# Kernel tuning notes

Measured on AMD Instinct MI355X. Metric: run time of the kernel, lower is better.

## Reference

```python
import jax, jax.numpy as jnp
import numpy as np

B, T, E, H = 8, 2048, 128, 4
FACTOR = 3  # autocorr_factor


def setup_inputs() -> dict:
    key = jax.random.key(0)
    ks = jax.random.split(key, 9)
    s = 0.05
    return {
        "hidden_states": jax.random.normal(ks[0], (B, T, E), jnp.float32),
        "wq": jax.random.normal(ks[1], (E, E, H), jnp.float32) * s,
        "bq": jax.random.normal(ks[2], (E, H), jnp.float32) * s,
        "wk": jax.random.normal(ks[3], (E, E, H), jnp.float32) * s,
        "bk": jax.random.normal(ks[4], (E, H), jnp.float32) * s,
        "wv": jax.random.normal(ks[5], (E, E, H), jnp.float32) * s,
        "bv": jax.random.normal(ks[6], (E, H), jnp.float32) * s,
        "wo": jax.random.normal(ks[7], (E, H, E), jnp.float32) * s,
        "bo": jax.random.normal(ks[8], (E,), jnp.float32) * s,
    }


def reference(hidden_states, wq, bq, wk, bk, wv, bv, wo, bo):
    # Inference path (training=None) of AutoCorrelation.call
    bsize, seq_len, _ = hidden_states.shape
    q = jnp.einsum('btj,juh->btuh', hidden_states, wq) + bq  # [B,T,E,H]
    k = jnp.einsum('btj,juh->btuh', hidden_states, wk) + bk
    v = jnp.einsum('btj,juh->btuh', hidden_states, wv) + bv

    # FFT cross-correlation over time axis
    qf = jnp.fft.rfft(q.transpose(0, 2, 3, 1), n=seq_len, axis=-1)  # [B,E,H,F]
    kf = jnp.fft.rfft(k.transpose(0, 2, 3, 1), n=seq_len, axis=-1)
    ac = jnp.fft.irfft(qf * jnp.conj(kf), n=seq_len, axis=-1)       # [B,E,H,T]
    ac = ac.transpose(0, 3, 1, 2)                                   # [B,T,E,H]

    ac_mean = ac.mean(axis=-1)                                      # [B,T,E]
    top_k = int(FACTOR * np.log(float(seq_len)))

    # top-k delays per (batch, channel)
    vals, idx = jax.lax.top_k(ac_mean.transpose(0, 2, 1), top_k)    # [B,E,K]
    w = jax.nn.softmax(vals, axis=-1)  # == Softmax(axis=-2) on [B,K,E]

    # NOTE: in the source, `delays_agg +=` is dedented outside the top_k loop,
    # so only the LAST iteration (i = top_k-1) contributes. Replicated faithfully.
    delay = idx[:, :, top_k - 1]   # [B,E] int
    wgt = w[:, :, top_k - 1]       # [B,E]

    # gather over doubled values == circular roll by -delay per (b, channel)
    t_idx = (jnp.arange(seq_len)[None, :, None] + delay[:, None, :]) % seq_len  # [B,T,E]
    rolled = jnp.take_along_axis(v, t_idx[..., None], axis=1)       # [B,T,E,H]
    agg = rolled * wgt[:, None, :, None]                            # [B,T,E,H]

    return jnp.einsum('btjh,jhf->btf', agg, wo) + bo                # [B,T,E]
```

## Files before the change

### kernel.cpp

```cpp
#include <hip/hip_runtime.h>
#include <math.h>

#define TSEQ 2048
#define BB 8
#define EE 128
#define HH 4
#define UHN 512
#define KTOP 22
#define BT (BB*TSEQ)
#define PITCH 76

typedef _Float16 f16;
typedef f16 f16x2 __attribute__((ext_vector_type(2)));
typedef f16 f16x4 __attribute__((ext_vector_type(4)));
typedef f16 f16x8 __attribute__((ext_vector_type(8)));
typedef float f32x4 __attribute__((ext_vector_type(4)));

__device__ __forceinline__ float2 cmul(float2 a, float2 b) {
  return make_float2(a.x*b.x - a.y*b.y, a.x*b.y + a.y*b.x);
}

__device__ __forceinline__ f16x8 ld_frag(const f16* p) {
  f16x4 lo = *(const f16x4*)(p);
  f16x4 hi = *(const f16x4*)(p + 16);
  return __builtin_shufflevector(lo, hi, 0, 1, 2, 3, 4, 5, 6, 7);
}

__global__ __launch_bounds__(256, 2)
void proj_mfma(const float* __restrict__ hs,
               const float* __restrict__ wq, const float* __restrict__ bq,
               const float* __restrict__ wk, const float* __restrict__ bk,
               const float* __restrict__ wv, const float* __restrict__ bv,
               float* __restrict__ q_t, float* __restrict__ k_t, float* __restrict__ v_t)
{
  __shared__ f16 Ah[128*PITCH];
  __shared__ f16 Al[128*PITCH];
  __shared__ f16 Bh[128*PITCH];
  __shared__ f16 Bl[128*PITCH];

  const float* W; const float* bias; float* outp;
  if (blockIdx.z == 0)      { W = wq; bias = bq; outp = q_t; }
  else if (blockIdx.z == 1) { W = wk; bias = bk; outp = k_t; }
  else                      { W = wv; bias = bv; outp = v_t; }

  const int tid  = threadIdx.x;
  const int lane = tid & 63, wid = tid >> 6;
  const int wm = wid >> 1, wn = wid & 1;
  const int ln15 = lane & 15, g = lane >> 4;
  const int uh0 = blockIdx.x * 128;
  const int bt0 = blockIdx.y * 128;

  f32x4 acc[4][4] = {};

  for (int kc = 0; kc < 2; ++kc) {
    const int k0 = kc * 64;
    __syncthreads();
#pragma unroll
    for (int r = 0; r < 16; ++r) {
      int idx = tid + 256*r;
      int u = idx & 127, kp = idx >> 7;
      float w0 = W[(size_t)(k0 + 2*kp    )*UHN + uh0 + u];
      float w1 = W[(size_t)(k0 + 2*kp + 1)*UHN + uh0 + u];
      f16 h0 = (f16)w0, h1 = (f16)w1;
      f16 l0 = (f16)(w0 - (float)h0), l1 = (f16)(w1 - (float)h1);
      *(f16x2*)&Ah[u*PITCH + 2*kp] = (f16x2){h0, h1};
      *(f16x2*)&Al[u*PITCH + 2*kp] = (f16x2){l0, l1};
    }
#pragma unroll
    for (int r = 0; r < 8; ++r) {
      int idx4 = tid + 256*r;
      int tl = idx4 >> 4, kq = idx4 & 15;
      float4 hv = *(const float4*)&hs[(size_t)(bt0 + tl)*EE + k0 + 4*kq];
      f16 h0 = (f16)hv.x, h1 = (f16)hv.y, h2 = (f16)hv.z, h3 = (f16)hv.w;
      *(f16x4*)&Bh[tl*PITCH + 4*kq] = (f16x4){h0, h1, h2, h3};
      *(f16x4*)&Bl[tl*PITCH + 4*kq] =
        (f16x4){(f16)(hv.x - (float)h0), (f16)(hv.y - (float)h1),
                (f16)(hv.z - (float)h2), (f16)(hv.w - (float)h3)};
    }
    __syncthreads();
#pragma unroll
    for (int ks = 0; ks < 2; ++ks) {
      const int kb = ks*32 + 4*g;
      f16x8 a_h[4], a_l[4], b_h[4], b_l[4];
#pragma unroll
      for (int mf = 0; mf < 4; ++mf) {
        int off = (wm*64 + mf*16 + ln15)*PITCH + kb;
        a_h[mf] = ld_frag(&Ah[off]);
        a_l[mf] = ld_frag(&Al[off]);
      }
#pragma unroll
      for (int nf = 0; nf < 4; ++nf) {
        int off = (wn*64 + nf*16 + ln15)*PITCH + kb;
        b_h[nf] = ld_frag(&Bh[off]);
        b_l[nf] = ld_frag(&Bl[off]);
      }
#pragma unroll
      for (int mf = 0; mf < 4; ++mf)
#pragma unroll
        for (int nf = 0; nf < 4; ++nf) {
          acc[mf][nf] = __builtin_amdgcn_mfma_f32_16x16x32_f16(a_h[mf], b_h[nf], acc[mf][nf], 0, 0, 0);
          acc[mf][nf] = __builtin_amdgcn_mfma_f32_16x16x32_f16(a_h[mf], b_l[nf], acc[mf][nf], 0, 0, 0);
          acc[mf][nf] = __builtin_amdgcn_mfma_f32_16x16x32_f16(a_l[mf], b_h[nf], acc[mf][nf], 0, 0, 0);
        }
    }
  }

  const int b = bt0 >> 11, tb = bt0 & (TSEQ - 1);
#pragma unroll
  for (int mf = 0; mf < 4; ++mf) {
    int uhb = uh0 + wm*64 + mf*16 + g*4;
    f32x4 bias4 = *(const f32x4*)&bias[uhb];
#pragma unroll
    for (int r = 0; r < 4; ++r) {
      size_t rowbase = ((size_t)(b*UHN + uhb + r))*TSEQ + tb;
#pragma unroll
      for (int nf = 0; nf < 4; ++nf) {
        int t = wn*64 + nf*16 + ln15;
        outp[rowbase + t] = acc[mf][nf][r] + bias4[r];
      }
    }
  }
}

__device__ __forceinline__ int brev11(int x) { return (int)(__brev((unsigned)x) >> 21); }

__global__ __launch_bounds__(256)
void fftcorr_kernel(const float* __restrict__ q_t, const float* __restrict__ k_t,
                    float* __restrict__ ac)
{
  __shared__ float2 bufZ[TSEQ];
  __shared__ float2 Sbuf[TSEQ];
  __shared__ float2 tw[TSEQ/2];

  const int tid = threadIdx.x;
  const int bu  = blockIdx.x;

#pragma unroll
  for (int r = 0; r < 4; ++r) {
    int j = tid + 256*r;
    float ang = -6.2831853071795864769f * (float)j / (float)TSEQ;
    float s, c;
    sincosf(ang, &s, &c);
    tw[j] = make_float2(c, s);
  }

  for (int h = 0; h < HH; ++h) {
    const float* qp = q_t + ((size_t)bu*HH + h)*TSEQ;
    const float* kp = k_t + ((size_t)bu*HH + h)*TSEQ;
    __syncthreads();
#pragma unroll
    for (int r = 0; r < 8; ++r) {
      int i = tid + 256*r;
      bufZ[i] = make_float2(qp[i], kp[i]);
    }
    int half = 1024, tws = 1;
    for (int st = 0; st < 11; ++st) {
      __syncthreads();
#pragma unroll
      for (int r = 0; r < 4; ++r) {
        int i = tid + 256*r;
        int j = i & (half - 1);
        int i0 = ((i - j) << 1) + j;
        int i1 = i0 + half;
        float2 w = tw[j * tws];
        float2 a = bufZ[i0], b2 = bufZ[i1];
        bufZ[i0] = make_float2(a.x + b2.x, a.y + b2.y);
        float2 d = make_float2(a.x - b2.x, a.y - b2.y);
        bufZ[i1] = cmul(d, w);
      }
      half >>= 1; tws <<= 1;
    }
    __syncthreads();
#pragma unroll
    for (int r = 0; r < 8; ++r) {
      int p = tid + 256*r;
      int kfreq = brev11(p);
      int pp = brev11((TSEQ - kfreq) & (TSEQ - 1));
      float2 A  = bufZ[p];
      float2 Zp = bufZ[pp];
      float re = 0.5f  * (Zp.x*A.y + Zp.y*A.x);
      float im = 0.25f * ((A.x*A.x + A.y*A.y) - (Zp.x*Zp.x + Zp.y*Zp.y));
      if (h == 0) Sbuf[p] = make_float2(re, im);
      else { Sbuf[p].x += re; Sbuf[p].y += im; }
    }
  }

  {
    int half = 1, tws = 1024;
    for (int st = 0; st < 11; ++st) {
      __syncthreads();
#pragma unroll
      for (int r = 0; r < 4; ++r) {
        int i = tid + 256*r;
        int j = i & (half - 1);
        int i0 = ((i - j) << 1) + j;
        int i1 = i0 + half;
        float2 w = tw[j * tws]; w.y = -w.y;
        float2 a = Sbuf[i0], b2 = Sbuf[i1];
        float2 t = cmul(b2, w);
        Sbuf[i0] = make_float2(a.x + t.x, a.y + t.y);
        Sbuf[i1] = make_float2(a.x - t.x, a.y - t.y);
      }
      half <<= 1; tws >>= 1;
    }
  }
  __syncthreads();

  const float scale = 1.0f / (float)(TSEQ * HH);
#pragma unroll
  for (int r = 0; r < 8; ++r) {
    int i = tid + 256*r;
    ac[(size_t)bu*TSEQ + i] = Sbuf[i].x * scale;
  }
}

__global__ __launch_bounds__(256)
void topk_kernel(const float* __restrict__ ac, int* __restrict__ delay,
                 float* __restrict__ wgt)
{
  __shared__ float v[TSEQ];
  __shared__ float rv[4];
  __shared__ int   ri[4];

  const int tid = threadIdx.x;
  const int bu  = blockIdx.x;

#pragma unroll
  for (int r = 0; r < 8; ++r) {
    int i = tid + 256*r;
    v[i] = ac[(size_t)bu*TSEQ + i];
  }

  float m0 = 0.f, ssum = 0.f;
  for (int it = 0; it < KTOP; ++it) {
    __syncthreads();
    float best = -3.4e38f; int bi = 0;
#pragma unroll
    for (int r = 0; r < 8; ++r) {
      int i = tid + 256*r;
      float x = v[i];
      if (x > best) { best = x; bi = i; }
    }
#pragma unroll
    for (int off = 32; off > 0; off >>= 1) {
      float ob = __shfl_down(best, off);
      int   oi = __shfl_down(bi, off);
      if (ob > best || (ob == best && oi < bi)) { best = ob; bi = oi; }
    }
    if ((tid & 63) == 0) { rv[tid >> 6] = best; ri[tid >> 6] = bi; }
    __syncthreads();
    if (tid == 0) {
      float gb = rv[0]; int gi = ri[0];
      for (int w2 = 1; w2 < 4; ++w2)
        if (rv[w2] > gb || (rv[w2] == gb && ri[w2] < gi)) { gb = rv[w2]; gi = ri[w2]; }
      v[gi] = -3.4e38f;
      if (it == 0) m0 = gb;
      ssum += expf(gb - m0);
      if (it == KTOP - 1) {
        delay[bu] = gi;
        wgt[bu]   = expf(gb - m0) / ssum;
      }
    }
  }
}

__global__ __launch_bounds__(256)
void out_mfma(const float* __restrict__ v_t, const int* __restrict__ delay,
              const float* __restrict__ wgt, const float* __restrict__ wo,
              const float* __restrict__ bo, float* __restrict__ out)
{
  __shared__ f16 Af[64*PITCH];
  __shared__ f16 Bf[64*PITCH];
  __shared__ int   dly[EE];
  __shared__ float wg[EE];

  const int tid  = threadIdx.x;
  const int lane = tid & 63, wid = tid >> 6;
  const int wm = wid >> 1, wn = wid & 1;
  const int ln15 = lane & 15, g = lane >> 4;
  const int t0g = blockIdx.x * 64;
  const int f0  = blockIdx.y * 64;
  const int b = t0g >> 11, t0 = t0g & (TSEQ - 1);

  if (tid < EE) { dly[tid] = delay[b*EE + tid]; wg[tid] = wgt[b*EE + tid]; }

  f32x4 acc[2][2] = {};

  for (int c = 0; c < 8; ++c) {
    const int uh0 = c * 64;
    __syncthreads();
#pragma unroll
    for (int r = 0; r < 16; ++r) {
      int idx = tid + 256*r;
      int tl = idx & 63, ul = idx >> 6;
      int u = (uh0 + ul) >> 2;
      float x = v_t[((size_t)(b*UHN + uh0 + ul))*TSEQ + ((t0 + tl + dly[u]) & (TSEQ-1))]
                * wg[u];
      Af[tl*PITCH + ul] = (f16)x;
    }
#pragma unroll
    for (int r = 0; r < 16; ++r) {
      int idx = tid + 256*r;
      int fl = idx & 63, ul = idx >> 6;
      Bf[fl*PITCH + ul] = (f16)wo[(size_t)(uh0 + ul)*EE + f0 + fl];
    }
    __syncthreads();
#pragma unroll
    for (int ks = 0; ks < 2; ++ks) {
      const int kb = ks*32 + 4*g;
      f16x8 av[2], bv[2];
#pragma unroll
      for (int mf = 0; mf < 2; ++mf)
        av[mf] = ld_frag(&Af[(wm*32 + mf*16 + ln15)*PITCH + kb]);
#pragma unroll
      for (int nf = 0; nf < 2; ++nf)
        bv[nf] = ld_frag(&Bf[(wn*32 + nf*16 + ln15)*PITCH + kb]);
#pragma unroll
      for (int mf = 0; mf < 2; ++mf)
#pragma unroll
        for (int nf = 0; nf < 2; ++nf)
          acc[mf][nf] = __builtin_amdgcn_mfma_f32_16x16x32_f16(av[mf], bv[nf], acc[mf][nf], 0, 0, 0);
    }
  }

#pragma unroll
  for (int mf = 0; mf < 2; ++mf)
#pragma unroll
    for (int r = 0; r < 4; ++r) {
      int bt = t0g + wm*32 + mf*16 + g*4 + r;
#pragma unroll
      for (int nf = 0; nf < 2; ++nf) {
        int f = f0 + wn*32 + nf*16 + ln15;
        out[(size_t)bt*EE + f] = acc[mf][nf][r] + bo[f];
      }
    }
}

extern "C" void kernel_launch(void* const* d_in, const int* in_sizes, int n_in,
                              void* d_out, int out_size, void* d_ws, size_t ws_size,
                              hipStream_t stream) {
  (void)in_sizes; (void)n_in; (void)out_size; (void)ws_size;
  const float* hs = (const float*)d_in[0];
  const float* wq = (const float*)d_in[1];
  const float* bq = (const float*)d_in[2];
  const float* wk = (const float*)d_in[3];
  const float* bk = (const float*)d_in[4];
  const float* wv = (const float*)d_in[5];
  const float* bv = (const float*)d_in[6];
  const float* wo = (const float*)d_in[7];
  const float* bo = (const float*)d_in[8];
  float* out = (float*)d_out;

  const size_t NQ = (size_t)BB * UHN * TSEQ;
  float* q_t = (float*)d_ws;
  float* k_t = q_t + NQ;
  float* v_t = k_t + NQ;
  float* ac  = v_t + NQ;
  int*   delay = (int*)(ac + (size_t)BB*EE*TSEQ);
  float* wgt   = (float*)(delay + BB*EE);

  proj_mfma<<<dim3(4, 128, 3), 256, 0, stream>>>(hs, wq, bq, wk, bk, wv, bv,
                                                 q_t, k_t, v_t);
  fftcorr_kernel<<<dim3(1024), 256, 0, stream>>>(q_t, k_t, ac);
  topk_kernel<<<dim3(1024), 256, 0, stream>>>(ac, delay, wgt);
  out_mfma<<<dim3(256, 2), 256, 0, stream>>>(v_t, delay, wgt, wo, bo, out);
}
```

Before: 141.9 us.

## Rewrite FFT correlation as radix-8/8/8/4 stages with padded shared memory

```diff
diff --git a/kernel.cpp b/kernel.cpp
--- a/kernel.cpp
+++ b/kernel.cpp
@@ -18,6 +18,12 @@
 
 __device__ __forceinline__ float2 cmul(float2 a, float2 b) {
   return make_float2(a.x*b.x - a.y*b.y, a.x*b.y + a.y*b.x);
+}
+__device__ __forceinline__ float2 cadd(float2 a, float2 b) {
+  return make_float2(a.x + b.x, a.y + b.y);
+}
+__device__ __forceinline__ float2 csub(float2 a, float2 b) {
+  return make_float2(a.x - b.x, a.y - b.y);
 }
 
 __device__ __forceinline__ f16x8 ld_frag(const f16* p) {
@@ -122,95 +128,194 @@
   }
 }
 
-__device__ __forceinline__ int brev11(int x) { return (int)(__brev((unsigned)x) >> 21); }
+#define ZPAD(g) ((g) + ((g) >> 5))
+
+template<int SGN>
+__device__ __forceinline__ float2 addim(float2 a, float2 b) {
+  return (SGN < 0) ? make_float2(a.x + b.y, a.y - b.x)
+                   : make_float2(a.x - b.y, a.y + b.x);
+}
+template<int SGN>
+__device__ __forceinline__ float2 subim(float2 a, float2 b) {
+  return (SGN < 0) ? make_float2(a.x - b.y, a.y + b.x)
+                   : make_float2(a.x + b.y, a.y - b.x);
+}
+
+template<int SGN>
+__device__ __forceinline__ void dft8(const float2* u, float2* y) {
+  const float r2 = 0.70710678118654752440f;
+  float2 a0 = cadd(u[0], u[4]), a1 = cadd(u[1], u[5]);
+  float2 a2 = cadd(u[2], u[6]), a3 = cadd(u[3], u[7]);
+  float2 b0 = csub(u[0], u[4]), b1 = csub(u[1], u[5]);
+  float2 b2 = csub(u[2], u[6]), b3 = csub(u[3], u[7]);
+  float2 t1 = (SGN < 0) ? make_float2(r2*(b1.x + b1.y), r2*(b1.y - b1.x))
+                        : make_float2(r2*(b1.x - b1.y), r2*(b1.y + b1.x));
+  float2 t2 = (SGN < 0) ? make_float2(b2.y, -b2.x) : make_float2(-b2.y, b2.x);
+  float2 e  = (SGN < 0) ? make_float2(r2*(b3.x + b3.y), r2*(b3.y - b3.x))
+                        : make_float2(r2*(b3.x - b3.y), r2*(b3.y + b3.x));
+  float2 t3 = (SGN < 0) ? make_float2(e.y, -e.x) : make_float2(-e.y, e.x);
+  {
+    float2 c0 = cadd(a0, a2), c1 = csub(a0, a2);
+    float2 c2 = cadd(a1, a3), c3 = csub(a1, a3);
+    y[0] = cadd(c0, c2); y[4] = csub(c0, c2);
+    y[2] = addim<SGN>(c1, c3); y[6] = subim<SGN>(c1, c3);
+  }
+  {
+    float2 c0 = cadd(b0, t2), c1 = csub(b0, t2);
+    float2 c2 = cadd(t1, t3), c3 = csub(t1, t3);
+    y[1] = cadd(c0, c2); y[5] = csub(c0, c2);
+    y[3] = addim<SGN>(c1, c3); y[7] = subim<SGN>(c1, c3);
+  }
+}
+
+__device__ __forceinline__ void fwd_radix8(float2* Z, float2 w1, int base, int eighth) {
+  float2 u[8];
+#pragma unroll
+  for (int t = 0; t < 8; ++t) u[t] = Z[ZPAD(base + eighth*t)];
+  float2 y[8];
+  dft8<-1>(u, y);
+  Z[ZPAD(base)] = y[0];
+  float2 w = w1;
+  Z[ZPAD(base + eighth)] = cmul(y[1], w);
+#pragma unroll
+  for (int s = 2; s < 8; ++s) {
+    w = cmul(w, w1);
+    Z[ZPAD(base + eighth*s)] = cmul(y[s], w);
+  }
+}
+
+__device__ __forceinline__ void inv_radix8(float2* Z, float2 w1c, int base, int eighth) {
+  float2 u[8];
+#pragma unroll
+  for (int t = 0; t < 8; ++t) u[t] = Z[ZPAD(base + eighth*t)];
+  u[1] = cmul(u[1], w1c);
+  float2 w = w1c;
+#pragma unroll
+  for (int t = 2; t < 8; ++t) {
+    w = cmul(w, w1c);
+    u[t] = cmul(u[t], w);
+  }
+  float2 y[8];
+  dft8<1>(u, y);
+#pragma unroll
+  for (int s = 0; s < 8; ++s) Z[ZPAD(base + eighth*s)] = y[s];
+}
+
+template<int SGN>
+__device__ __forceinline__ void radix4_stage(float2* Z, int base) {
+  float2 v0 = Z[ZPAD(base)], v1 = Z[ZPAD(base+1)];
+  float2 v2 = Z[ZPAD(base+2)], v3 = Z[ZPAD(base+3)];
+  float2 c0 = cadd(v0, v2), c1 = csub(v0, v2);
+  float2 c2 = cadd(v1, v3), c3 = csub(v1, v3);
+  Z[ZPAD(base)]   = cadd(c0, c2);
+  Z[ZPAD(base+1)] = addim<SGN>(c1, c3);
+  Z[ZPAD(base+2)] = csub(c0, c2);
+  Z[ZPAD(base+3)] = subim<SGN>(c1, c3);
+}
 
 __global__ __launch_bounds__(256)
 void fftcorr_kernel(const float* __restrict__ q_t, const float* __restrict__ k_t,
                     float* __restrict__ ac)
 {
-  __shared__ float2 bufZ[TSEQ];
-  __shared__ float2 Sbuf[TSEQ];
-  __shared__ float2 tw[TSEQ/2];
+  __shared__ float2 Z[2112];
+  __shared__ float2 twl[292];
 
   const int tid = threadIdx.x;
   const int bu  = blockIdx.x;
 
-#pragma unroll
-  for (int r = 0; r < 4; ++r) {
-    int j = tid + 256*r;
-    float ang = -6.2831853071795864769f * (float)j / (float)TSEQ;
+  for (int idx = tid; idx < 292; idx += 256) {
+    float ang;
+    if (idx < 256)      ang = -6.2831853071795864769f * (float)idx / 2048.0f;
+    else if (idx < 288) ang = -6.2831853071795864769f * (float)(idx - 256) / 256.0f;
+    else                ang = -6.2831853071795864769f * (float)(idx - 288) / 32.0f;
     float s, c;
     sincosf(ang, &s, &c);
-    tw[j] = make_float2(c, s);
-  }
+    twl[idx] = make_float2(c, s);
+  }
+  const float2* tw1 = twl;
+  const float2* tw2 = twl + 256;
+  const float2* tw3 = twl + 288;
+
+  int pp[8];
+#pragma unroll
+  for (int r = 0; r < 8; ++r) {
+    int p = tid + (r << 8);
+    int f = ((p >> 8) & 7) | (((p >> 5) & 7) << 3) | (((p >> 2) & 7) << 6) | ((p & 3) << 9);
+    int nf = (2048 - f) & 2047;
+    pp[r] = ((nf & 7) << 8) | (((nf >> 3) & 7) << 5) | (((nf >> 6) & 7) << 2) | ((nf >> 9) & 3);
+  }
+  float2 sreg[8] = {};
+  __syncthreads();
 
   for (int h = 0; h < HH; ++h) {
     const float* qp = q_t + ((size_t)bu*HH + h)*TSEQ;
     const float* kp = k_t + ((size_t)bu*HH + h)*TSEQ;
+    {
+      float2 u[8];
+#pragma unroll
+      for (int t = 0; t < 8; ++t)
+        u[t] = make_float2(qp[tid + 256*t], kp[tid + 256*t]);
+      float2 y[8];
+      dft8<-1>(u, y);
+      float2 w1 = tw1[tid];
+      Z[ZPAD(tid)] = y[0];
+      float2 w = w1;
+      Z[ZPAD(tid + 256)] = cmul(y[1], w);
+#pragma unroll
+      for (int s = 2; s < 8; ++s) {
+        w = cmul(w, w1);
+        Z[ZPAD(tid + 256*s)] = cmul(y[s], w);
+      }
+    }
+    __syncthreads();
+    fwd_radix8(Z, tw2[tid & 31], ((tid >> 5) << 8) + (tid & 31), 32);
+    __syncthreads();
+    fwd_radix8(Z, tw3[tid & 3], ((tid >> 2) << 5) + (tid & 3), 4);
+    __syncthreads();
+    radix4_stage<-1>(Z, 4*tid);
+    radix4_stage<-1>(Z, 4*(tid + 256));
     __syncthreads();
 #pragma unroll
     for (int r = 0; r < 8; ++r) {
-      int i = tid + 256*r;
-      bufZ[i] = make_float2(qp[i], kp[i]);
-    }
-    int half = 1024, tws = 1;
-    for (int st = 0; st < 11; ++st) {
-      __syncthreads();
-#pragma unroll
-      for (int r = 0; r < 4; ++r) {
-        int i = tid + 256*r;
-        int j = i & (half - 1);
-        int i0 = ((i - j) << 1) + j;
-        int i1 = i0 + half;
-        float2 w = tw[j * tws];
-        float2 a = bufZ[i0], b2 = bufZ[i1];
-        bufZ[i0] = make_float2(a.x + b2.x, a.y + b2.y);
-        float2 d = make_float2(a.x - b2.x, a.y - b2.y);
-        bufZ[i1] = cmul(d, w);
-      }
-      half >>= 1; tws <<= 1;
-    }
-    __syncthreads();
-#pragma unroll
-    for (int r = 0; r < 8; ++r) {
-      int p = tid + 256*r;
-      int kfreq = brev11(p);
-      int pp = brev11((TSEQ - kfreq) & (TSEQ - 1));
-      float2 A  = bufZ[p];
-      float2 Zp = bufZ[pp];
-      float re = 0.5f  * (Zp.x*A.y + Zp.y*A.x);
-      float im = 0.25f * ((A.x*A.x + A.y*A.y) - (Zp.x*Zp.x + Zp.y*Zp.y));
-      if (h == 0) Sbuf[p] = make_float2(re, im);
-      else { Sbuf[p].x += re; Sbuf[p].y += im; }
-    }
-  }
-
+      int p = tid + (r << 8);
+      float2 A  = Z[ZPAD(p)];
+      float2 Zp = Z[ZPAD(pp[r])];
+      sreg[r].x += 0.5f  * (Zp.x*A.y + Zp.y*A.x);
+      sreg[r].y += 0.25f * ((A.x*A.x + A.y*A.y) - (Zp.x*Zp.x + Zp.y*Zp.y));
+    }
+    __syncthreads();
+  }
+
+#pragma unroll
+  for (int r = 0; r < 8; ++r) Z[ZPAD(tid + (r << 8))] = sreg[r];
+  __syncthreads();
+  radix4_stage<1>(Z, 4*tid);
+  radix4_stage<1>(Z, 4*(tid + 256));
+  __syncthreads();
+  { float2 w = tw3[tid & 3]; w.y = -w.y;
+    inv_radix8(Z, w, ((tid >> 2) << 5) + (tid & 3), 4); }
+  __syncthreads();
+  { float2 w = tw2[tid & 31]; w.y = -w.y;
+    inv_radix8(Z, w, ((tid >> 5) << 8) + (tid & 31), 32); }
+  __syncthreads();
   {
-    int half = 1, tws = 1024;
-    for (int st = 0; st < 11; ++st) {
-      __syncthreads();
-#pragma unroll
-      for (int r = 0; r < 4; ++r) {
-        int i = tid + 256*r;
-        int j = i & (half - 1);
-        int i0 = ((i - j) << 1) + j;
-        int i1 = i0 + half;
-        float2 w = tw[j * tws]; w.y = -w.y;
-        float2 a = Sbuf[i0], b2 = Sbuf[i1];
-        float2 t = cmul(b2, w);
-        Sbuf[i0] = make_float2(a.x + t.x, a.y + t.y);
-        Sbuf[i1] = make_float2(a.x - t.x, a.y - t.y);
-      }
-      half <<= 1; tws >>= 1;
-    }
-  }
-  __syncthreads();
-
-  const float scale = 1.0f / (float)(TSEQ * HH);
-#pragma unroll
-  for (int r = 0; r < 8; ++r) {
-    int i = tid + 256*r;
-    ac[(size_t)bu*TSEQ + i] = Sbuf[i].x * scale;
+    float2 u[8];
+#pragma unroll
+    for (int t = 0; t < 8; ++t) u[t] = Z[ZPAD(tid + 256*t)];
+    float2 w1c = tw1[tid]; w1c.y = -w1c.y;
+    u[1] = cmul(u[1], w1c);
+    float2 w = w1c;
+#pragma unroll
+    for (int t = 2; t < 8; ++t) {
+      w = cmul(w, w1c);
+      u[t] = cmul(u[t], w);
+    }
+    float2 y[8];
+    dft8<1>(u, y);
+    const float scale = 1.0f / (float)(TSEQ * HH);
+#pragma unroll
+    for (int s = 0; s < 8; ++s)
+      ac[(size_t)bu*TSEQ + tid + 256*s] = y[s].x * scale;
   }
 }
 
```

Result: faster. 116.6 us (-17.8%).
